# Performance work log

Measured on AMD Instinct MI355X. Metric: run time of the kernel, lower is better.

The kernel has to match this reference:

```python
import jax, jax.numpy as jnp
import numpy as np
import math

H = 16          # attention heads
NH = 4          # lact (fast-weight) heads
CHUNK = 1024    # lact_chunk_size
WIN = 1024      # sliding window
ROPE_THETA = 500000.0
BASE_LR_INV = 0.001 + math.log(-math.expm1(-0.001))  # inv_softplus(1e-3)


def rmsnorm(x, w, eps=1e-6):
    return x * jax.lax.rsqrt(jnp.mean(x * x, axis=-1, keepdims=True) + eps) * w


def rope(x, cos, sin):
    # x: [b, s, h, d]; cos/sin: [s, d//2]; non-interleaved (rotate-half) convention
    d2 = x.shape[-1] // 2
    x1, x2 = x[..., :d2], x[..., d2:]
    c = cos[None, :, None, :]
    s_ = sin[None, :, None, :]
    return jnp.concatenate([x1 * c - x2 * s_, x2 * c + x1 * s_], axis=-1)


def setup_inputs() -> dict:
    key = jax.random.key(0)
    b, s, d = 2, 2048, 2048
    fd = d // NH          # fw head dim = 512
    dh = fd               # inter_multi = 1.0
    ks = jax.random.split(key, 12)
    return {
        "hidden_states": jax.random.normal(ks[0], (b, s, d), jnp.float32),
        "Wqkv": jax.random.normal(ks[1], (3 * d, d), jnp.float32) / math.sqrt(d),
        "Wo": jax.random.normal(ks[2], (d, d), jnp.float32) / math.sqrt(d),
        "q_norm_w": jnp.ones((d,), jnp.float32),
        "k_norm_w": jnp.ones((d,), jnp.float32),
        "w0": jax.random.normal(ks[3], (NH, dh, fd), jnp.float32) / math.sqrt(fd),
        "w1": jax.random.normal(ks[4], (NH, fd, dh), jnp.float32) / math.sqrt(dh),
        "w2": jax.random.normal(ks[5], (NH, dh, fd), jnp.float32) / math.sqrt(fd),
        "lr_w": jax.random.normal(ks[6], (3 * NH, d), jnp.float32) * 0.02,
        "lr_b": jnp.zeros((3 * NH,), jnp.float32),
        "qk_scale": jnp.ones((d, 2), jnp.float32),
        "qk_offset": jnp.zeros((d, 2), jnp.float32),
        "ttt_norm_w": jnp.ones((fd,), jnp.float32),
    }


def reference(hidden_states, Wqkv, Wo, q_norm_w, k_norm_w, w0, w1, w2,
              lr_w, lr_b, qk_scale, qk_offset, ttt_norm_w):
    b, s, d = hidden_states.shape
    hd = d // H   # attn head dim
    fd = d // NH  # fw head dim

    qkv = hidden_states @ Wqkv.T
    q, k, v = jnp.split(qkv, 3, axis=-1)

    # ---------- sliding-window causal attention with RoPE ----------
    aq = rmsnorm(q, q_norm_w).reshape(b, s, H, hd)
    ak = rmsnorm(k, k_norm_w).reshape(b, s, H, hd)
    av = v.reshape(b, s, H, hd)
    inv_freq = 1.0 / (ROPE_THETA ** (jnp.arange(0, hd, 2, dtype=jnp.float32) / hd))
    ang = jnp.arange(s, dtype=jnp.float32)[:, None] * inv_freq[None, :]
    cos, sin = jnp.cos(ang), jnp.sin(ang)
    aq = rope(aq, cos, sin)
    ak = rope(ak, cos, sin)
    scores = jnp.einsum('bqhd,bkhd->bhqk', aq, ak) / math.sqrt(hd)
    i = jnp.arange(s)[:, None]
    j = jnp.arange(s)[None, :]
    mask = (j <= i) & (i - j < WIN)
    scores = jnp.where(mask[None, None], scores, -jnp.inf)
    p = jax.nn.softmax(scores, axis=-1)
    attn_out = jnp.einsum('bhqk,bkhd->bqhd', p, av).reshape(b, s, d)

    # ---------- LaCT fast-weight SwiGLU path (chunked update-then-apply) ----------
    fq = jax.nn.silu(q) * qk_scale[:, 0] + qk_offset[:, 0]
    fk = jax.nn.silu(k) * qk_scale[:, 1] + qk_offset[:, 1]
    fv = jax.nn.silu(v)
    fq = fq.reshape(b, s, NH, fd)
    fk = fk.reshape(b, s, NH, fd)
    fv = fv.reshape(b, s, NH, fd)
    # l2-normalize q/k per fw head
    fq = fq / (jnp.linalg.norm(fq, axis=-1, keepdims=True) + 1e-12)
    fk = fk / (jnp.linalg.norm(fk, axis=-1, keepdims=True) + 1e-12)
    # per-token per-head learning rates (mamba parameterization)
    lr = jax.nn.softplus(hidden_states @ lr_w.T + lr_b + BASE_LR_INV)  # [b,s,3*NH]
    lr0, lr1, lr2 = jnp.split(lr, 3, axis=-1)  # each [b,s,NH]

    nC = s // CHUNK
    BH = b * NH

    def to_chunks(x):  # [b,s,NH,fd] -> [nC, BH, CHUNK, fd]
        return x.transpose(0, 2, 1, 3).reshape(BH, nC, CHUNK, x.shape[-1]).transpose(1, 0, 2, 3)

    def lr_chunks(x):  # [b,s,NH] -> [nC, BH, CHUNK, 1]
        return x.transpose(0, 2, 1).reshape(BH, nC, CHUNK, 1).transpose(1, 0, 2, 3)

    qc, kc, vc = to_chunks(fq), to_chunks(fk), to_chunks(fv)
    l0, l1, l2 = lr_chunks(lr0), lr_chunks(lr1), lr_chunks(lr2)

    w0b = jnp.tile(w0, (b, 1, 1))  # [BH, dh, fd]
    w1b = jnp.tile(w1, (b, 1, 1))  # [BH, fd, dh]
    w2b = jnp.tile(w2, (b, 1, 1))  # [BH, dh, fd]

    def step(carry, xs):
        w0c, w1c, w2c = carry
        qi, ki, vi, li0, li1, li2 = xs
        # forward of fast net on keys
        gate = jnp.einsum('bcd,bhd->bch', ki, w0c)        # [BH,C,dh]
        hpre = jnp.einsum('bcd,bhd->bch', ki, w2c)
        hid = jax.nn.silu(gate) * hpre
        # gradient of dot-product loss  L = -sum v . f(k)  (descent direction, positive sign)
        dh_ = jnp.einsum('bco,boh->bch', vi, w1c)         # w1^T v
        dhpre = dh_ * jax.nn.silu(gate)
        sig = jax.nn.sigmoid(gate)
        dgate = dh_ * hpre * (sig * (1.0 + gate * (1.0 - sig)))
        # per-token lr-weighted updates
        w0n = w0c + jnp.einsum('bch,bcd->bhd', dgate * li0, ki)
        w2n = w2c + jnp.einsum('bch,bcd->bhd', dhpre * li2, ki)
        w1n = w1c + jnp.einsum('bco,bch->boh', vi * li1, hid)
        # apply updated fast weights to queries of this chunk
        gq = jnp.einsum('bcd,bhd->bch', qi, w0n)
        hq = jax.nn.silu(gq) * jnp.einsum('bcd,bhd->bch', qi, w2n)
        oi = jnp.einsum('bch,boh->bco', hq, w1n)
        return (w0n, w1n, w2n), oi

    _, out_c = jax.lax.scan(step, (w0b, w1b, w2b), (qc, kc, vc, l0, l1, l2))
    # [nC,BH,C,fd] -> [b,s,NH,fd]
    ttt = out_c.transpose(1, 0, 2, 3).reshape(b, NH, s, fd).transpose(0, 2, 1, 3)
    ttt = rmsnorm(ttt, ttt_norm_w).reshape(b, s, d)

    return (attn_out + ttt) @ Wo.T
```

## Files before the change

kernel.cpp:

```cpp
#include <hip/hip_runtime.h>
#include <hip/hip_bf16.h>
#include <math.h>

#define S 2048
#define NH 4
#define FD 512
#define CHUNK 1024
#define BASE_LR_INV -6.9072552373f

typedef unsigned short u16;
typedef unsigned int u32;
typedef short bhalf8 __attribute__((ext_vector_type(8)));
typedef float floatx4 __attribute__((ext_vector_type(4)));

__device__ __forceinline__ u16 f2bf(float f) {
    u32 x = __float_as_uint(f);
    return (u16)((x + 0x7FFFu + ((x >> 16) & 1u)) >> 16);
}
__device__ __forceinline__ float bf2f(u16 u) {
    return __uint_as_float(((u32)u) << 16);
}
__device__ __forceinline__ float ldval(const float* p) { return *p; }
__device__ __forceinline__ float ldval(const u16* p) { return bf2f(*p); }

__device__ __forceinline__ void gl_lds16(const u16* g, u16* l)
{
    __builtin_amdgcn_global_load_lds(
        (const __attribute__((address_space(1))) void*)g,
        (__attribute__((address_space(3))) void*)l, 16, 0, 0);
}

__global__ __launch_bounds__(256) void gemm_mfma(
    const u16* __restrict__ A, int lda, long offAo, long offAi,
    const u16* __restrict__ B, int ldb, long offBo, long offBi,
    float* __restrict__ C, int ldc, long offCo, long offCi, int K, int acc_flag)
{
    int z = blockIdx.z;
    A += (long)(z >> 2) * offAo + (long)(z & 3) * offAi;
    B += (long)(z >> 2) * offBo + (long)(z & 3) * offBi;
    C += (long)(z >> 2) * offCo + (long)(z & 3) * offCi;
    __shared__ u16 As0[128][32], Bs0[128][32];
    __shared__ u16 As1[128][32], Bs1[128][32];
    const int tid = threadIdx.x;
    const int wid = tid >> 6, lane = tid & 63;
    const int quad = lane >> 4, l15 = lane & 15;
    const int m0w = (wid >> 1) * 64, n0w = (wid & 1) * 64;
    const int row0 = blockIdx.y * 128, col0 = blockIdx.x * 128;
    const int srow = lane >> 2, scol = (lane & 3) * 8;
    const int ca = wid * 16, cb = (wid + 4) * 16;

    const u16* gA0 = &A[(long)(row0 + ca + srow) * lda + scol];
    const u16* gA1 = &A[(long)(row0 + cb + srow) * lda + scol];
    const u16* gB0 = &B[(long)(col0 + ca + srow) * ldb + scol];
    const u16* gB1 = &B[(long)(col0 + cb + srow) * ldb + scol];

    floatx4 acc[4][4];
#pragma unroll
    for (int a = 0; a < 4; ++a)
#pragma unroll
        for (int b = 0; b < 4; ++b) acc[a][b] = {0.f, 0.f, 0.f, 0.f};

#define GSTAGE(AS, BS, kk) do { \
    gl_lds16(gA0 + (kk), &AS[ca][0]); \
    gl_lds16(gA1 + (kk), &AS[cb][0]); \
    gl_lds16(gB0 + (kk), &BS[ca][0]); \
    gl_lds16(gB1 + (kk), &BS[cb][0]); } while (0)

#define GCOMP(AS, BS) do { \
    bhalf8 af[4], bf[4]; \
    _Pragma("unroll") \
    for (int mt = 0; mt < 4; ++mt) \
        af[mt] = *reinterpret_cast<const bhalf8*>(&AS[m0w + mt * 16 + l15][quad * 8]); \
    _Pragma("unroll") \
    for (int nt = 0; nt < 4; ++nt) \
        bf[nt] = *reinterpret_cast<const bhalf8*>(&BS[n0w + nt * 16 + l15][quad * 8]); \
    _Pragma("unroll") \
    for (int mt = 0; mt < 4; ++mt) \
        _Pragma("unroll") \
        for (int nt = 0; nt < 4; ++nt) \
            acc[mt][nt] = __builtin_amdgcn_mfma_f32_16x16x32_bf16( \
                af[mt], bf[nt], acc[mt][nt], 0, 0, 0); } while (0)

    const int nt = K >> 5;
    GSTAGE(As0, Bs0, 0);
    for (int t = 0; t < nt; t += 2) {
        __syncthreads();
        GSTAGE(As1, Bs1, (t + 1) * 32);
        GCOMP(As0, Bs0);
        __syncthreads();
        if (t + 2 < nt) GSTAGE(As0, Bs0, (t + 2) * 32);
        GCOMP(As1, Bs1);
    }
#undef GSTAGE
#undef GCOMP

#pragma unroll
    for (int mt = 0; mt < 4; ++mt)
#pragma unroll
        for (int nt = 0; nt < 4; ++nt) {
            int col = col0 + n0w + nt * 16 + l15;
#pragma unroll
            for (int r = 0; r < 4; ++r) {
                int row = row0 + m0w + mt * 16 + quad * 4 + r;
                long off = (long)row * ldc + col;
                float v = acc[mt][nt][r];
                C[off] = acc_flag ? (C[off] + v) : v;
            }
        }
}

__global__ __launch_bounds__(256) void gemm_mfma64(
    const u16* __restrict__ A, int lda, long offAo, long offAi,
    const u16* __restrict__ B, int ldb, long offBo, long offBi,
    float* __restrict__ C, int ldc, long offCo, long offCi, int K, int acc_flag)
{
    int z = blockIdx.z;
    A += (long)(z >> 2) * offAo + (long)(z & 3) * offAi;
    B += (long)(z >> 2) * offBo + (long)(z & 3) * offBi;
    C += (long)(z >> 2) * offCo + (long)(z & 3) * offCi;
    __shared__ u16 As0[64][32], Bs0[64][32];
    __shared__ u16 As1[64][32], Bs1[64][32];
    const int tid = threadIdx.x;
    const int wid = tid >> 6, lane = tid & 63;
    const int quad = lane >> 4, l15 = lane & 15;
    const int m0w = (wid >> 1) * 32, n0w = (wid & 1) * 32;
    const int row0 = blockIdx.y * 64, col0 = blockIdx.x * 64;
    const int srow = lane >> 2, scol = (lane & 3) * 8;
    const int ca = wid * 16;

    const u16* gA0 = &A[(long)(row0 + ca + srow) * lda + scol];
    const u16* gB0 = &B[(long)(col0 + ca + srow) * ldb + scol];

    floatx4 acc[2][2];
#pragma unroll
    for (int a = 0; a < 2; ++a)
#pragma unroll
        for (int b = 0; b < 2; ++b) acc[a][b] = {0.f, 0.f, 0.f, 0.f};

#define GSTAGE64(AS, BS, kk) do { \
    gl_lds16(gA0 + (kk), &AS[ca][0]); \
    gl_lds16(gB0 + (kk), &BS[ca][0]); } while (0)

#define GCOMP64(AS, BS) do { \
    bhalf8 af[2], bf[2]; \
    _Pragma("unroll") \
    for (int mt = 0; mt < 2; ++mt) \
        af[mt] = *reinterpret_cast<const bhalf8*>(&AS[m0w + mt * 16 + l15][quad * 8]); \
    _Pragma("unroll") \
    for (int nt = 0; nt < 2; ++nt) \
        bf[nt] = *reinterpret_cast<const bhalf8*>(&BS[n0w + nt * 16 + l15][quad * 8]); \
    _Pragma("unroll") \
    for (int mt = 0; mt < 2; ++mt) \
        _Pragma("unroll") \
        for (int nt = 0; nt < 2; ++nt) \
            acc[mt][nt] = __builtin_amdgcn_mfma_f32_16x16x32_bf16( \
                af[mt], bf[nt], acc[mt][nt], 0, 0, 0); } while (0)

    const int nt = K >> 5;
    GSTAGE64(As0, Bs0, 0);
    for (int t = 0; t < nt; t += 2) {
        __syncthreads();
        GSTAGE64(As1, Bs1, (t + 1) * 32);
        GCOMP64(As0, Bs0);
        __syncthreads();
        if (t + 2 < nt) GSTAGE64(As0, Bs0, (t + 2) * 32);
        GCOMP64(As1, Bs1);
    }
#undef GSTAGE64
#undef GCOMP64

#pragma unroll
    for (int mt = 0; mt < 2; ++mt)
#pragma unroll
        for (int nt = 0; nt < 2; ++nt) {
            int col = col0 + n0w + nt * 16 + l15;
#pragma unroll
            for (int r = 0; r < 4; ++r) {
                int row = row0 + m0w + mt * 16 + quad * 4 + r;
                long off = (long)row * ldc + col;
                float v = acc[mt][nt][r];
                C[off] = acc_flag ? (C[off] + v) : v;
            }
        }
}

__global__ __launch_bounds__(256) void cvt_bf16(
    const float* __restrict__ in, u16* __restrict__ out, long n)
{
    long i = ((long)blockIdx.x * 256 + threadIdx.x) * 4;
    if (i >= n) return;
    float4 v = *reinterpret_cast<const float4*>(&in[i]);
    ushort4 o;
    o.x = f2bf(v.x); o.y = f2bf(v.y); o.z = f2bf(v.z); o.w = f2bf(v.w);
    *reinterpret_cast<ushort4*>(&out[i]) = o;
}

__global__ __launch_bounds__(256) void cvt_pack(
    const float* __restrict__ in, u16* __restrict__ out, int half)
{
    long idx = ((long)blockIdx.x * 256 + threadIdx.x) * 4;
    int col = (int)(idx & 511);
    long r = idx >> 9;
    int row = (int)(r & 511);
    int z = (int)(r >> 9);
    float4 v = *reinterpret_cast<const float4*>(&in[idx]);
    ushort4 o;
    o.x = f2bf(v.x); o.y = f2bf(v.y); o.z = f2bf(v.z); o.w = f2bf(v.w);
    long dst = ((long)z * 1024 + half * 512 + row) * 512 + col;
    *reinterpret_cast<ushort4*>(&out[dst]) = o;
}

template <typename TIN>
__global__ __launch_bounds__(256) void transpose_cvt(
    const TIN* __restrict__ in, int ldin, long inOo, long inOi,
    u16* __restrict__ out, int ldout, long outOo, long outOi)
{
    int z = blockIdx.z;
    in  += (long)(z >> 2) * inOo + (long)(z & 3) * inOi;
    out += (long)(z >> 2) * outOo + (long)(z & 3) * outOi;
    int r0 = blockIdx.y * 64, c0 = blockIdx.x * 64;
    __shared__ float t[64][65];
    for (int i = threadIdx.x; i < 4096; i += 256) {
        int r = i >> 6, c = i & 63;
        t[r][c] = ldval(&in[(long)(r0 + r) * ldin + c0 + c]);
    }
    __syncthreads();
    for (int i = threadIdx.x; i < 4096; i += 256) {
        int r = i >> 6, c = i & 63;
        out[(long)(c0 + r) * ldout + r0 + c] = f2bf(t[c][r]);
    }
}

__global__ __launch_bounds__(256) void transpose_cvt2(
    const float* __restrict__ inA, const float* __restrict__ inB, int ldin, long inOi,
    u16* __restrict__ outA, u16* __restrict__ outB, int ldout, long outOi)
{
    int zz = blockIdx.z;
    int z = zz & 7, sel = zz >> 3;
    const float* in = (sel ? inB : inA) + (long)z * inOi;
    u16* out = (sel ? outB : outA) + (long)z * outOi;
    int r0 = blockIdx.y * 64, c0 = blockIdx.x * 64;
    __shared__ float t[64][65];
    for (int i = threadIdx.x; i < 4096; i += 256) {
        int r = i >> 6, c = i & 63;
        t[r][c] = in[(long)(r0 + r) * ldin + c0 + c];
    }
    __syncthreads();
    for (int i = threadIdx.x; i < 4096; i += 256) {
        int r = i >> 6, c = i & 63;
        out[(long)(c0 + r) * ldout + r0 + c] = f2bf(t[c][r]);
    }
}

__global__ __launch_bounds__(256) void vt_prep(
    const float* __restrict__ qkv, u16* __restrict__ vt)
{
    int z = blockIdx.z;
    int b_ = z >> 4, h = z & 15;
    int s0 = blockIdx.x * 64, d0 = blockIdx.y * 64;
    __shared__ float t[64][65];
    const float* src = &qkv[(long)(b_ * S) * 6144 + 4096 + h * 128 + d0];
    for (int i = threadIdx.x; i < 4096; i += 256) {
        int r = i >> 6, c = i & 63;
        t[r][c] = src[(long)(s0 + r) * 6144 + c];
    }
    __syncthreads();
    u16* dst = &vt[((long)z * 128 + d0) * 2048 + s0];
    for (int i = threadIdx.x; i < 4096; i += 256) {
        int r = i >> 6, c = i & 63;
        dst[(long)r * 2048 + c] = f2bf(t[c][r]);
    }
}

__global__ __launch_bounds__(256) void lr_kernel(
    const float* __restrict__ hs, const float* __restrict__ lr_w,
    const float* __restrict__ lr_b, float* __restrict__ lr)
{
    int row = blockIdx.x;
    __shared__ float hrow[2048];
    for (int i = threadIdx.x; i < 2048; i += 256) hrow[i] = hs[(long)row * 2048 + i];
    __syncthreads();
    int wid = threadIdx.x >> 6, lane = threadIdx.x & 63;
    for (int j = wid; j < 12; j += 4) {
        const float* wrow = &lr_w[(long)j * 2048];
        float ss = 0.f;
        for (int i = lane; i < 2048; i += 64) ss += hrow[i] * wrow[i];
#pragma unroll
        for (int off = 32; off > 0; off >>= 1) ss += __shfl_down(ss, off);
        if (lane == 0) {
            float x = ss + lr_b[j] + BASE_LR_INV;
            lr[(long)row * 12 + j] = (x > 20.f) ? x : log1pf(expf(x));
        }
    }
}

__global__ __launch_bounds__(256) void rmsnorm_rope(
    const float* __restrict__ qkv, int colOff, const float* __restrict__ w,
    u16* __restrict__ out)
{
    int row = blockIdx.x;
    int si = row & (S - 1);
    const float* x = &qkv[(long)row * 6144 + colOff];
    __shared__ float xn[2048];
    __shared__ float red[256];
    __shared__ float cst[64], snt[64];
    if (threadIdx.x < 64) {
        float inv_freq = powf(500000.0f, -(float)threadIdx.x / 64.0f);
        float ang = (float)si * inv_freq;
        float sn, cs;
        sincosf(ang, &sn, &cs);
        cst[threadIdx.x] = cs;
        snt[threadIdx.x] = sn;
    }
    float ss = 0.f;
    for (int i = threadIdx.x; i < 2048; i += 256) { float v = x[i]; ss += v * v; }
    red[threadIdx.x] = ss; __syncthreads();
    for (int s_ = 128; s_ > 0; s_ >>= 1) {
        if (threadIdx.x < s_) red[threadIdx.x] += red[threadIdx.x + s_];
        __syncthreads();
    }
    float scale = rsqrtf(red[0] / 2048.f + 1e-6f);
    for (int i = threadIdx.x; i < 2048; i += 256) xn[i] = x[i] * scale * w[i];
    __syncthreads();
    for (int i = threadIdx.x; i < 2048; i += 256) {
        int tt = i & 127;
        int t2 = tt & 63;
        float cs = cst[t2], sn = snt[t2];
        float v;
        if (tt < 64) v = xn[i] * cs - xn[i + 64] * sn;
        else         v = xn[i] * cs + xn[i - 64] * sn;
        out[(long)row * 2048 + i] = f2bf(v);
    }
}

__global__ __launch_bounds__(256) void attn_mfma(
    const u16* __restrict__ aq, const u16* __restrict__ ak,
    const u16* __restrict__ vt, float* __restrict__ attn_out)
{
    const int qt = blockIdx.x;
    const int h  = blockIdx.y;
    const int b_ = blockIdx.z;
    const int q0 = qt * 64;
    const int tid = threadIdx.x;
    const int wid = tid >> 6, lane = tid & 63;
    const int quad = lane >> 4, l15 = lane & 15;
    const int m0w = (wid >> 1) * 32;
    const int n0w = (wid & 1) * 32;
    const int n0v = (wid & 1) * 64;
    const float scale = 0.088388347648318447f;

    __shared__ u16  Ks[64][136];
    __shared__ float Ss[64][67];
    __shared__ u16  Ps[64][72];
    __shared__ u16  Vs[128][72];
    __shared__ float alphas[64];
    __shared__ float lsum[64];

    const long qkbase = (long)(b_ * S + q0) * 2048 + h * 128;
    const long vtbase = ((long)(b_ * 16 + h)) * 128 * 2048;

    {
        int r = tid >> 2, c = (tid & 3) * 32;
        const u16* g = &aq[qkbase + (long)r * 2048 + c];
#pragma unroll
        for (int o = 0; o < 32; o += 8)
            *reinterpret_cast<uint4*>(&Ks[r][c + o]) = *reinterpret_cast<const uint4*>(g + o);
    }
    __syncthreads();
    bhalf8 qf[2][4];
#pragma unroll
    for (int mt = 0; mt < 2; ++mt)
#pragma unroll
        for (int ks = 0; ks < 4; ++ks)
            qf[mt][ks] = *reinterpret_cast<const bhalf8*>(&Ks[m0w + mt * 16 + l15][ks * 32 + quad * 8]);
    __syncthreads();

    floatx4 oacc[2][4];
#pragma unroll
    for (int mt = 0; mt < 2; ++mt)
#pragma unroll
        for (int nt = 0; nt < 4; ++nt) oacc[mt][nt] = {0.f, 0.f, 0.f, 0.f};
    float m_i = -3.4e38f, l_i = 0.f;
    const int srow_sm = tid >> 2, scol_sm = (tid & 3) * 16;

    const int st = (qt >= 16) ? (qt - 16) : 0;
    for (int kt = st; kt <= qt; ++kt) {
        const int j0 = kt * 64;
        {
            int r = tid >> 2, c = (tid & 3) * 32;
            const u16* g = &ak[(long)(b_ * S + j0) * 2048 + h * 128 + (long)r * 2048 + c];
#pragma unroll
            for (int o = 0; o < 32; o += 8)
                *reinterpret_cast<uint4*>(&Ks[r][c + o]) = *reinterpret_cast<const uint4*>(g + o);
        }
        {
            int r = tid >> 1, c = (tid & 1) * 32;
            const u16* g = &vt[vtbase + (long)r * 2048 + j0 + c];
#pragma unroll
            for (int o = 0; o < 32; o += 8)
                *reinterpret_cast<uint4*>(&Vs[r][c + o]) = *reinterpret_cast<const uint4*>(g + o);
        }
        __syncthreads();

        floatx4 sacc[2][2];
#pragma unroll
        for (int mt = 0; mt < 2; ++mt)
#pragma unroll
            for (int nt = 0; nt < 2; ++nt) sacc[mt][nt] = {0.f, 0.f, 0.f, 0.f};
#pragma unroll
        for (int ks = 0; ks < 4; ++ks) {
            bhalf8 kf0 = *reinterpret_cast<const bhalf8*>(&Ks[n0w + l15][ks * 32 + quad * 8]);
            bhalf8 kf1 = *reinterpret_cast<const bhalf8*>(&Ks[n0w + 16 + l15][ks * 32 + quad * 8]);
            sacc[0][0] = __builtin_amdgcn_mfma_f32_16x16x32_bf16(qf[0][ks], kf0, sacc[0][0], 0, 0, 0);
            sacc[0][1] = __builtin_amdgcn_mfma_f32_16x16x32_bf16(qf[0][ks], kf1, sacc[0][1], 0, 0, 0);
            sacc[1][0] = __builtin_amdgcn_mfma_f32_16x16x32_bf16(qf[1][ks], kf0, sacc[1][0], 0, 0, 0);
            sacc[1][1] = __builtin_amdgcn_mfma_f32_16x16x32_bf16(qf[1][ks], kf1, sacc[1][1], 0, 0, 0);
        }
#pragma unroll
        for (int mt = 0; mt < 2; ++mt)
#pragma unroll
            for (int nt = 0; nt < 2; ++nt)
#pragma unroll
                for (int r = 0; r < 4; ++r) {
                    int row = m0w + mt * 16 + quad * 4 + r;
                    int col = n0w + nt * 16 + l15;
                    int i_abs = q0 + row, j_abs = j0 + col;
                    bool valid = (j_abs <= i_abs) && (i_abs - j_abs < 1024);
                    Ss[row][col] = valid ? sacc[mt][nt][r] * scale : -3.4e38f;
                }
        __syncthreads();

        {
            float sv[16];
            float mx = -3.4e38f;
#pragma unroll
            for (int j = 0; j < 16; ++j) {
                sv[j] = Ss[srow_sm][scol_sm + j];
                mx = fmaxf(mx, sv[j]);
            }
            mx = fmaxf(mx, __shfl_xor(mx, 1));
            mx = fmaxf(mx, __shfl_xor(mx, 2));
            float m_new = fmaxf(m_i, mx);
            float alpha = expf(m_i - m_new);
            float psum = 0.f;
#pragma unroll
            for (int j = 0; j < 16; ++j) {
                float p = (sv[j] > -1e30f) ? expf(sv[j] - m_new) : 0.f;
                Ps[srow_sm][scol_sm + j] = f2bf(p);
                psum += p;
            }
            psum += __shfl_xor(psum, 1);
            psum += __shfl_xor(psum, 2);
            l_i = l_i * alpha + psum;
            m_i = m_new;
            if ((tid & 3) == 0) alphas[srow_sm] = alpha;
        }
        __syncthreads();

#pragma unroll
        for (int mt = 0; mt < 2; ++mt)
#pragma unroll
            for (int r = 0; r < 4; ++r) {
                float al = alphas[m0w + mt * 16 + quad * 4 + r];
#pragma unroll
                for (int nt = 0; nt < 4; ++nt) oacc[mt][nt][r] *= al;
            }
#pragma unroll
        for (int ks = 0; ks < 2; ++ks) {
            bhalf8 pf0 = *reinterpret_cast<const bhalf8*>(&Ps[m0w + l15][ks * 32 + quad * 8]);
            bhalf8 pf1 = *reinterpret_cast<const bhalf8*>(&Ps[m0w + 16 + l15][ks * 32 + quad * 8]);
#pragma unroll
            for (int nt = 0; nt < 4; ++nt) {
                bhalf8 vf = *reinterpret_cast<const bhalf8*>(&Vs[n0v + nt * 16 + l15][ks * 32 + quad * 8]);
                oacc[0][nt] = __builtin_amdgcn_mfma_f32_16x16x32_bf16(pf0, vf, oacc[0][nt], 0, 0, 0);
                oacc[1][nt] = __builtin_amdgcn_mfma_f32_16x16x32_bf16(pf1, vf, oacc[1][nt], 0, 0, 0);
            }
        }
        __syncthreads();
    }

    if ((tid & 3) == 0) lsum[srow_sm] = l_i;
    __syncthreads();
#pragma unroll
    for (int mt = 0; mt < 2; ++mt)
#pragma unroll
        for (int r = 0; r < 4; ++r) {
            int row = m0w + mt * 16 + quad * 4 + r;
            float inv = 1.0f / lsum[row];
#pragma unroll
            for (int nt = 0; nt < 4; ++nt)
                attn_out[qkbase + (long)row * 2048 + n0v + nt * 16 + l15] = oacc[mt][nt][r] * inv;
        }
}

__global__ __launch_bounds__(128) void fqkv_kernel(
    const float* __restrict__ qkv, const float* __restrict__ qk_scale,
    const float* __restrict__ qk_offset, u16* __restrict__ fq,
    u16* __restrict__ fk, u16* __restrict__ fv)
{
    int mode = blockIdx.y;
    int bid = blockIdx.x;
    int nh = bid & 3;
    int row = bid >> 2;
    const float* x = &qkv[(long)row * 6144 + mode * 2048 + nh * 512];
    __shared__ float red[128];
    float vals[4];
    float ss = 0.f;
#pragma unroll
    for (int ii = 0; ii < 4; ++ii) {
        int i = threadIdx.x + ii * 128;
        float v = x[i];
        float sg = 1.f / (1.f + expf(-v));
        float sv = v * sg;
        if (mode < 2) {
            int dcol = nh * 512 + i;
            sv = sv * qk_scale[dcol * 2 + mode] + qk_offset[dcol * 2 + mode];
        }
        vals[ii] = sv;
        ss += sv * sv;
    }
    float invn = 1.0f;
    if (mode < 2) {
        red[threadIdx.x] = ss; __syncthreads();
        for (int s_ = 64; s_ > 0; s_ >>= 1) {
            if (threadIdx.x < s_) red[threadIdx.x] += red[threadIdx.x + s_];
            __syncthreads();
        }
        invn = 1.0f / (sqrtf(red[0]) + 1e-12f);
    }
    u16* base = (mode == 0) ? fq : (mode == 1) ? fk : fv;
    u16* o = &base[(long)row * 2048 + nh * 512];
#pragma unroll
    for (int ii = 0; ii < 4; ++ii) o[threadIdx.x + ii * 128] = f2bf(vals[ii] * invn);
}

__global__ void winit(const float* __restrict__ w0, const float* __restrict__ w1,
                      const float* __restrict__ w2, float* __restrict__ w0b,
                      float* __restrict__ w1b, float* __restrict__ w2b)
{
    long idx = (long)blockIdx.x * 256 + threadIdx.x;
    long src = ((idx >> 18) & 3) * 262144 + (idx & 262143);
    w0b[idx] = w0[src];
    w1b[idx] = w1[src];
    w2b[idx] = w2[src];
}

__global__ void scan_ew1(float* T12, float* T3, const u16* fvb,
                         const float* lr, int c0, float* T4)
{
    long idx = (long)blockIdx.x * 256 + threadIdx.x;
    int f = (int)(idx & 511);
    long r = idx >> 9;
    int ci = (int)(r & 1023);
    int z = (int)(r >> 10);
    int b_ = z >> 2, h = z & 3;
    long srow = (long)b_ * S + (long)c0 * CHUNK + ci;
    long base12 = r * 1024;
    float g = T12[base12 + f];
    float hp = T12[base12 + 512 + f];
    float dh = T3[idx];
    float sg = 1.f / (1.f + expf(-g));
    float silu_g = g * sg;
    float hid = silu_g * hp;
    float dgate = dh * hp * (sg * (1.f + g * (1.f - sg)));
    float dhpre = dh * silu_g;
    float l0 = lr[srow * 12 + h];
    float l1 = lr[srow * 12 + 4 + h];
    float l2 = lr[srow * 12 + 8 + h];
    float fvv = bf2f(fvb[srow * 2048 + h * 512 + f]);
    T12[base12 + f] = dgate * l0;
    T12[base12 + 512 + f] = dhpre * l2;
    T3[idx] = fvv * l1;
    T4[idx] = hid;
}

__global__ void scan_ew2c(const float* __restrict__ T12, u16* __restrict__ hq)
{
    long idx = (long)blockIdx.x * 256 + threadIdx.x;
    int f = (int)(idx & 511);
    long r = idx >> 9;
    long base12 = r * 1024;
    float g = T12[base12 + f];
    float h2 = T12[base12 + 512 + f];
    float v = g * (1.f / (1.f + expf(-g))) * h2;
    hq[idx] = f2bf(v);
}

__global__ __launch_bounds__(128) void ttt_norm_add(
    const float* __restrict__ ttt, const float* __restrict__ w, float* attnX)
{
    int bid = blockIdx.x;
    int h = bid & 3;
    int row = bid >> 2;
    const float* x = &ttt[(long)row * 2048 + h * 512];
    __shared__ float red[128];
    float v[4];
    float ss = 0.f;
#pragma unroll
    for (int ii = 0; ii < 4; ++ii) {
        v[ii] = x[threadIdx.x + ii * 128];
        ss += v[ii] * v[ii];
    }
    red[threadIdx.x] = ss; __syncthreads();
    for (int s_ = 64; s_ > 0; s_ >>= 1) {
        if (threadIdx.x < s_) red[threadIdx.x] += red[threadIdx.x + s_];
        __syncthreads();
    }
    float sc = rsqrtf(red[0] / 512.f + 1e-6f);
    float* o = &attnX[(long)row * 2048 + h * 512];
#pragma unroll
    for (int ii = 0; ii < 4; ++ii) {
        int i = threadIdx.x + ii * 128;
        o[i] = o[i] + v[ii] * sc * w[i];
    }
}

extern "C" void kernel_launch(void* const* d_in, const int* in_sizes, int n_in,
                              void* d_out, int out_size, void* d_ws, size_t ws_size,
                              hipStream_t stream)
{
    const float* hs        = (const float*)d_in[0];
    const float* Wqkv      = (const float*)d_in[1];
    const float* Wo        = (const float*)d_in[2];
    const float* q_norm_w  = (const float*)d_in[3];
    const float* k_norm_w  = (const float*)d_in[4];
    const float* w0        = (const float*)d_in[5];
    const float* w1        = (const float*)d_in[6];
    const float* w2        = (const float*)d_in[7];
    const float* lr_w      = (const float*)d_in[8];
    const float* lr_b      = (const float*)d_in[9];
    const float* qk_scale  = (const float*)d_in[10];
    const float* qk_offset = (const float*)d_in[11];
    const float* ttt_w     = (const float*)d_in[12];
    float* out = (float*)d_out;
    float* ws = (float*)d_ws;

    const long F_QKV = 0;
    const long F_TTT = 0;
    const long F_T1  = 8388608;
    const long F_T3  = 16777216;
    const long F_T4  = 20971520;
    const long F_AQ  = 25165824;
    const long F_AK  = 33554432;
    const long F_ATT = 41943040;
    const long F_TTa = 50331648;
    const long F_TTb = 52428800;
    const long F_W0  = 54525952;
    const long F_W1  = 56623104;
    const long F_W2  = 58720256;
    const long F_W02B= 60817408;
    const long F_W1B = 62914560;
    const long F_W1T = 63963136;
    const long F_LR  = 65011712;

    u16* hs_b   = (u16*)(ws + F_AQ);
    u16* wqkv_b = (u16*)(ws + F_AK);
    u16* aq_b   = (u16*)(ws + F_AQ);
    u16* ak_b   = (u16*)(ws + F_AK);
    u16* vt_b   = (u16*)(ws + F_AQ + 4194304);
    u16* fq_b   = (u16*)(ws + F_AQ);
    u16* fk_b   = (u16*)(ws + F_AQ + 4194304);
    u16* fv_b   = (u16*)(ws + F_AK);
    u16* hq_b   = (u16*)(ws + F_AK + 4194304);
    u16* fkt_b  = (u16*)(ws + F_AK + 6291456);
    u16* tta    = (u16*)(ws + F_TTa);
    u16* ttb    = (u16*)(ws + F_TTb);
    u16* w02b_u = (u16*)(ws + F_W02B);
    u16* w1b_u  = (u16*)(ws + F_W1B);
    u16* w1t_u  = (u16*)(ws + F_W1T);
    u16* x_b    = (u16*)(ws + F_T1);
    u16* wo_b   = (u16*)(ws + F_T3);

    cvt_bf16<<<8192, 256, 0, stream>>>(hs, hs_b, 8388608);
    cvt_bf16<<<12288, 256, 0, stream>>>(Wqkv, wqkv_b, 12582912);
    gemm_mfma<<<dim3(48, 32, 1), 256, 0, stream>>>(
        hs_b, 2048, 0, 0, wqkv_b, 2048, 0, 0, ws + F_QKV, 6144, 0, 0, 2048, 0);
    lr_kernel<<<4096, 256, 0, stream>>>(hs, lr_w, lr_b, ws + F_LR);
    rmsnorm_rope<<<4096, 256, 0, stream>>>(ws + F_QKV, 0,    q_norm_w, aq_b);
    rmsnorm_rope<<<4096, 256, 0, stream>>>(ws + F_QKV, 2048, k_norm_w, ak_b);
    vt_prep<<<dim3(32, 2, 32), 256, 0, stream>>>(ws + F_QKV, vt_b);
    attn_mfma<<<dim3(32, 16, 2), 256, 0, stream>>>(aq_b, ak_b, vt_b, ws + F_ATT);
    fqkv_kernel<<<dim3(16384, 3), 128, 0, stream>>>(
        ws + F_QKV, qk_scale, qk_offset, fq_b, fk_b, fv_b);
    winit<<<8192, 256, 0, stream>>>(w0, w1, w2, ws + F_W0, ws + F_W1, ws + F_W2);

    for (int c0 = 0; c0 < 2; ++c0) {
        const long cOff = (long)c0 * 2097152;
        cvt_pack<<<2048, 256, 0, stream>>>(ws + F_W0, w02b_u, 0);
        cvt_pack<<<2048, 256, 0, stream>>>(ws + F_W2, w02b_u, 1);
        transpose_cvt<float><<<dim3(8, 8, 8), 256, 0, stream>>>(
            ws + F_W1, 512, 1048576, 262144, w1t_u, 512, 1048576, 262144);
        transpose_cvt<u16><<<dim3(8, 16, 8), 256, 0, stream>>>(
            fk_b + cOff, 2048, 4194304, 512, fkt_b, 1024, 2097152, 524288);
        gemm_mfma<<<dim3(8, 8, 8), 256, 0, stream>>>(
            fk_b + cOff, 2048, 4194304, 512, w02b_u, 512, 2097152, 524288,
            ws + F_T1, 1024, 4194304, 1048576, 512, 0);
        gemm_mfma<<<dim3(4, 8, 8), 256, 0, stream>>>(
            fv_b + cOff, 2048, 4194304, 512, w1t_u, 512, 1048576, 262144,
            ws + F_T3, 512, 2097152, 524288, 512, 0);
        scan_ew1<<<16384, 256, 0, stream>>>(ws + F_T1, ws + F_T3, fv_b,
                                            ws + F_LR, c0, ws + F_T4);
        transpose_cvt2<<<dim3(8, 16, 16), 256, 0, stream>>>(
            ws + F_T1, ws + F_T1 + 512, 1024, 1048576, tta, ttb, 1024, 524288);
        gemm_mfma64<<<dim3(8, 8, 8), 256, 0, stream>>>(
            tta, 1024, 2097152, 524288, fkt_b, 1024, 2097152, 524288,
            ws + F_W0, 512, 1048576, 262144, 1024, 1);
        gemm_mfma64<<<dim3(8, 8, 8), 256, 0, stream>>>(
            ttb, 1024, 2097152, 524288, fkt_b, 1024, 2097152, 524288,
            ws + F_W2, 512, 1048576, 262144, 1024, 1);
        transpose_cvt2<<<dim3(8, 16, 16), 256, 0, stream>>>(
            ws + F_T3, ws + F_T4, 512, 524288, tta, ttb, 1024, 524288);
        gemm_mfma64<<<dim3(8, 8, 8), 256, 0, stream>>>(
            tta, 1024, 2097152, 524288, ttb, 1024, 2097152, 524288,
            ws + F_W1, 512, 1048576, 262144, 1024, 1);
        cvt_pack<<<2048, 256, 0, stream>>>(ws + F_W0, w02b_u, 0);
        cvt_pack<<<2048, 256, 0, stream>>>(ws + F_W2, w02b_u, 1);
        cvt_bf16<<<2048, 256, 0, stream>>>(ws + F_W1, w1b_u, 2097152);
        gemm_mfma<<<dim3(8, 8, 8), 256, 0, stream>>>(
            fq_b + cOff, 2048, 4194304, 512, w02b_u, 512, 2097152, 524288,
            ws + F_T1, 1024, 4194304, 1048576, 512, 0);
        scan_ew2c<<<16384, 256, 0, stream>>>(ws + F_T1, hq_b);
        gemm_mfma<<<dim3(4, 8, 8), 256, 0, stream>>>(
            hq_b, 512, 2097152, 524288, w1b_u, 512, 1048576, 262144,
            ws + F_TTT + cOff, 2048, 4194304, 512, 512, 0);
    }

    ttt_norm_add<<<16384, 128, 0, stream>>>(ws + F_TTT, ttt_w, ws + F_ATT);
    cvt_bf16<<<8192, 256, 0, stream>>>(ws + F_ATT, x_b, 8388608);
    cvt_bf16<<<4096, 256, 0, stream>>>(Wo, wo_b, 4194304);
    gemm_mfma<<<dim3(16, 32, 1), 256, 0, stream>>>(
        x_b, 2048, 0, 0, wo_b, 2048, 0, 0, out, 2048, 0, 0, 2048, 0);
}
```

Measured before the change: 1.007 ms.

## Fuse scan elementwise with transposes, fuse ttt norm with bf16 cast, swizzle GEMM blocks

Merges the chunk-update elementwise kernel with both transpose-convert passes into one tiled kernel that writes the four bf16 transposed operands directly through LDS. This removes two launches and the fp32 round trips through T12/T3/T4 per chunk. It also folds the final ttt rmsnorm-add into the bf16 conversion of the Wo GEMM input, dropping a read-write pass. All MFMA GEMMs now remap workgroup IDs so that consecutive tiles land on the same XCD, aiming for better L2 locality, at the cost of some index arithmetic per block.

```diff
diff --git a/kernel.cpp b/kernel.cpp
--- a/kernel.cpp
+++ b/kernel.cpp
@@ -30,12 +30,29 @@
         (__attribute__((address_space(3))) void*)l, 16, 0, 0);
 }
 
+__device__ __forceinline__ void xcd_swizzle(int& bx, int& by, int& bz)
+{
+    long gx = gridDim.x, gy = gridDim.y;
+    long nwg = gx * gy * gridDim.z;
+    long flat = blockIdx.x + gx * (blockIdx.y + gy * blockIdx.z);
+    if ((nwg & 7) == 0) {
+        long cpx = nwg >> 3;
+        flat = (flat & 7) * cpx + (flat >> 3);
+    }
+    bx = (int)(flat % gx);
+    long t = flat / gx;
+    by = (int)(t % gy);
+    bz = (int)(t / gy);
+}
+
 __global__ __launch_bounds__(256) void gemm_mfma(
     const u16* __restrict__ A, int lda, long offAo, long offAi,
     const u16* __restrict__ B, int ldb, long offBo, long offBi,
     float* __restrict__ C, int ldc, long offCo, long offCi, int K, int acc_flag)
 {
-    int z = blockIdx.z;
+    int bx, by, bz;
+    xcd_swizzle(bx, by, bz);
+    int z = bz;
     A += (long)(z >> 2) * offAo + (long)(z & 3) * offAi;
     B += (long)(z >> 2) * offBo + (long)(z & 3) * offBi;
     C += (long)(z >> 2) * offCo + (long)(z & 3) * offCi;
@@ -45,7 +62,7 @@
     const int wid = tid >> 6, lane = tid & 63;
     const int quad = lane >> 4, l15 = lane & 15;
     const int m0w = (wid >> 1) * 64, n0w = (wid & 1) * 64;
-    const int row0 = blockIdx.y * 128, col0 = blockIdx.x * 128;
+    const int row0 = by * 128, col0 = bx * 128;
     const int srow = lane >> 2, scol = (lane & 3) * 8;
     const int ca = wid * 16, cb = (wid + 4) * 16;
 
@@ -114,7 +131,9 @@
     const u16* __restrict__ B, int ldb, long offBo, long offBi,
     float* __restrict__ C, int ldc, long offCo, long offCi, int K, int acc_flag)
 {
-    int z = blockIdx.z;
+    int bx, by, bz;
+    xcd_swizzle(bx, by, bz);
+    int z = bz;
     A += (long)(z >> 2) * offAo + (long)(z & 3) * offAi;
     B += (long)(z >> 2) * offBo + (long)(z & 3) * offBi;
     C += (long)(z >> 2) * offCo + (long)(z & 3) * offCi;
@@ -124,7 +143,7 @@
     const int wid = tid >> 6, lane = tid & 63;
     const int quad = lane >> 4, l15 = lane & 15;
     const int m0w = (wid >> 1) * 32, n0w = (wid & 1) * 32;
-    const int row0 = blockIdx.y * 64, col0 = blockIdx.x * 64;
+    const int row0 = by * 64, col0 = bx * 64;
     const int srow = lane >> 2, scol = (lane & 3) * 8;
     const int ca = wid * 16;
 
@@ -231,27 +250,6 @@
     }
 }
 
-__global__ __launch_bounds__(256) void transpose_cvt2(
-    const float* __restrict__ inA, const float* __restrict__ inB, int ldin, long inOi,
-    u16* __restrict__ outA, u16* __restrict__ outB, int ldout, long outOi)
-{
-    int zz = blockIdx.z;
-    int z = zz & 7, sel = zz >> 3;
-    const float* in = (sel ? inB : inA) + (long)z * inOi;
-    u16* out = (sel ? outB : outA) + (long)z * outOi;
-    int r0 = blockIdx.y * 64, c0 = blockIdx.x * 64;
-    __shared__ float t[64][65];
-    for (int i = threadIdx.x; i < 4096; i += 256) {
-        int r = i >> 6, c = i & 63;
-        t[r][c] = in[(long)(r0 + r) * ldin + c0 + c];
-    }
-    __syncthreads();
-    for (int i = threadIdx.x; i < 4096; i += 256) {
-        int r = i >> 6, c = i & 63;
-        out[(long)(c0 + r) * ldout + r0 + c] = f2bf(t[c][r]);
-    }
-}
-
 __global__ __launch_bounds__(256) void vt_prep(
     const float* __restrict__ qkv, u16* __restrict__ vt)
 {
@@ -545,33 +543,58 @@
     w2b[idx] = w2[src];
 }
 
-__global__ void scan_ew1(float* T12, float* T3, const u16* fvb,
-                         const float* lr, int c0, float* T4)
-{
-    long idx = (long)blockIdx.x * 256 + threadIdx.x;
-    int f = (int)(idx & 511);
-    long r = idx >> 9;
-    int ci = (int)(r & 1023);
-    int z = (int)(r >> 10);
+__global__ __launch_bounds__(256) void scan_ew1t(
+    const float* __restrict__ T12, const float* __restrict__ T3,
+    const u16* __restrict__ fvb, const float* __restrict__ lr, int c0,
+    u16* __restrict__ ta, u16* __restrict__ tb,
+    u16* __restrict__ tc, u16* __restrict__ td)
+{
+    int f0 = blockIdx.x * 64, ci0 = blockIdx.y * 64, z = blockIdx.z;
     int b_ = z >> 2, h = z & 3;
-    long srow = (long)b_ * S + (long)c0 * CHUNK + ci;
-    long base12 = r * 1024;
-    float g = T12[base12 + f];
-    float hp = T12[base12 + 512 + f];
-    float dh = T3[idx];
-    float sg = 1.f / (1.f + expf(-g));
-    float silu_g = g * sg;
-    float hid = silu_g * hp;
-    float dgate = dh * hp * (sg * (1.f + g * (1.f - sg)));
-    float dhpre = dh * silu_g;
-    float l0 = lr[srow * 12 + h];
-    float l1 = lr[srow * 12 + 4 + h];
-    float l2 = lr[srow * 12 + 8 + h];
-    float fvv = bf2f(fvb[srow * 2048 + h * 512 + f]);
-    T12[base12 + f] = dgate * l0;
-    T12[base12 + 512 + f] = dhpre * l2;
-    T3[idx] = fvv * l1;
-    T4[idx] = hid;
+    __shared__ u16 la[64][66], lb[64][66], lc[64][66], ldt[64][66];
+    const int tr = threadIdx.x >> 4, tc4 = (threadIdx.x & 15) * 4;
+#pragma unroll
+    for (int it = 0; it < 4; ++it) {
+        int r = tr + it * 16;
+        long row = (long)z * 1024 + ci0 + r;
+        long srow = (long)b_ * S + (long)c0 * CHUNK + ci0 + r;
+        float4 g4  = *reinterpret_cast<const float4*>(&T12[row * 1024 + f0 + tc4]);
+        float4 hp4 = *reinterpret_cast<const float4*>(&T12[row * 1024 + 512 + f0 + tc4]);
+        float4 dh4 = *reinterpret_cast<const float4*>(&T3[row * 512 + f0 + tc4]);
+        ushort4 fv4 = *reinterpret_cast<const ushort4*>(&fvb[srow * 2048 + h * 512 + f0 + tc4]);
+        float l0 = lr[srow * 12 + h];
+        float l1 = lr[srow * 12 + 4 + h];
+        float l2 = lr[srow * 12 + 8 + h];
+        float gs[4]  = {g4.x, g4.y, g4.z, g4.w};
+        float hps[4] = {hp4.x, hp4.y, hp4.z, hp4.w};
+        float dhs[4] = {dh4.x, dh4.y, dh4.z, dh4.w};
+        u16 fvs[4]   = {fv4.x, fv4.y, fv4.z, fv4.w};
+#pragma unroll
+        for (int j = 0; j < 4; ++j) {
+            float g = gs[j], hp = hps[j], dh = dhs[j];
+            float sg = 1.f / (1.f + expf(-g));
+            float silu_g = g * sg;
+            la[r][tc4 + j]  = f2bf(dh * hp * (sg * (1.f + g * (1.f - sg))) * l0);
+            lb[r][tc4 + j]  = f2bf(dh * silu_g * l2);
+            lc[r][tc4 + j]  = f2bf(bf2f(fvs[j]) * l1);
+            ldt[r][tc4 + j] = f2bf(silu_g * hp);
+        }
+    }
+    __syncthreads();
+#pragma unroll
+    for (int it = 0; it < 4; ++it) {
+        int r = tr + it * 16;
+        long obase = ((long)z * 512 + f0 + r) * 1024 + ci0 + tc4;
+        ushort4 va, vb, vc, vd;
+        va.x = la[tc4][r];  va.y = la[tc4+1][r];  va.z = la[tc4+2][r];  va.w = la[tc4+3][r];
+        vb.x = lb[tc4][r];  vb.y = lb[tc4+1][r];  vb.z = lb[tc4+2][r];  vb.w = lb[tc4+3][r];
+        vc.x = lc[tc4][r];  vc.y = lc[tc4+1][r];  vc.z = lc[tc4+2][r];  vc.w = lc[tc4+3][r];
+        vd.x = ldt[tc4][r]; vd.y = ldt[tc4+1][r]; vd.z = ldt[tc4+2][r]; vd.w = ldt[tc4+3][r];
+        *reinterpret_cast<ushort4*>(&ta[obase]) = va;
+        *reinterpret_cast<ushort4*>(&tb[obase]) = vb;
+        *reinterpret_cast<ushort4*>(&tc[obase]) = vc;
+        *reinterpret_cast<ushort4*>(&td[obase]) = vd;
+    }
 }
 
 __global__ void scan_ew2c(const float* __restrict__ T12, u16* __restrict__ hq)
@@ -586,8 +609,9 @@
     hq[idx] = f2bf(v);
 }
 
-__global__ __launch_bounds__(128) void ttt_norm_add(
-    const float* __restrict__ ttt, const float* __restrict__ w, float* attnX)
+__global__ __launch_bounds__(128) void ttt_norm_cvt(
+    const float* __restrict__ ttt, const float* __restrict__ w,
+    const float* __restrict__ attnX, u16* __restrict__ xb)
 {
     int bid = blockIdx.x;
     int h = bid & 3;
@@ -607,11 +631,12 @@
         __syncthreads();
     }
     float sc = rsqrtf(red[0] / 512.f + 1e-6f);
-    float* o = &attnX[(long)row * 2048 + h * 512];
+    const float* a = &attnX[(long)row * 2048 + h * 512];
+    u16* o = &xb[(long)row * 2048 + h * 512];
 #pragma unroll
     for (int ii = 0; ii < 4; ++ii) {
         int i = threadIdx.x + ii * 128;
-        o[i] = o[i] + v[ii] * sc * w[i];
+        o[i] = f2bf(a[i] + v[ii] * sc * w[i]);
     }
 }
 
@@ -639,7 +664,8 @@
     const long F_TTT = 0;
     const long F_T1  = 8388608;
     const long F_T3  = 16777216;
-    const long F_T4  = 20971520;
+    const long F_TC  = 20971520;
+    const long F_TD  = 23068672;
     const long F_AQ  = 25165824;
     const long F_AK  = 33554432;
     const long F_ATT = 41943040;
@@ -665,6 +691,8 @@
     u16* fkt_b  = (u16*)(ws + F_AK + 6291456);
     u16* tta    = (u16*)(ws + F_TTa);
     u16* ttb    = (u16*)(ws + F_TTb);
+    u16* ttc    = (u16*)(ws + F_TC);
+    u16* ttd    = (u16*)(ws + F_TD);
     u16* w02b_u = (u16*)(ws + F_W02B);
     u16* w1b_u  = (u16*)(ws + F_W1B);
     u16* w1t_u  = (u16*)(ws + F_W1T);
@@ -698,20 +726,16 @@
         gemm_mfma<<<dim3(4, 8, 8), 256, 0, stream>>>(
             fv_b + cOff, 2048, 4194304, 512, w1t_u, 512, 1048576, 262144,
             ws + F_T3, 512, 2097152, 524288, 512, 0);
-        scan_ew1<<<16384, 256, 0, stream>>>(ws + F_T1, ws + F_T3, fv_b,
-                                            ws + F_LR, c0, ws + F_T4);
-        transpose_cvt2<<<dim3(8, 16, 16), 256, 0, stream>>>(
-            ws + F_T1, ws + F_T1 + 512, 1024, 1048576, tta, ttb, 1024, 524288);
+        scan_ew1t<<<dim3(8, 16, 8), 256, 0, stream>>>(
+            ws + F_T1, ws + F_T3, fv_b, ws + F_LR, c0, tta, ttb, ttc, ttd);
         gemm_mfma64<<<dim3(8, 8, 8), 256, 0, stream>>>(
             tta, 1024, 2097152, 524288, fkt_b, 1024, 2097152, 524288,
             ws + F_W0, 512, 1048576, 262144, 1024, 1);
         gemm_mfma64<<<dim3(8, 8, 8), 256, 0, stream>>>(
             ttb, 1024, 2097152, 524288, fkt_b, 1024, 2097152, 524288,
             ws + F_W2, 512, 1048576, 262144, 1024, 1);
-        transpose_cvt2<<<dim3(8, 16, 16), 256, 0, stream>>>(
-            ws + F_T3, ws + F_T4, 512, 524288, tta, ttb, 1024, 524288);
         gemm_mfma64<<<dim3(8, 8, 8), 256, 0, stream>>>(
-            tta, 1024, 2097152, 524288, ttb, 1024, 2097152, 524288,
+            ttc, 1024, 2097152, 524288, ttd, 1024, 2097152, 524288,
             ws + F_W1, 512, 1048576, 262144, 1024, 1);
         cvt_pack<<<2048, 256, 0, stream>>>(ws + F_W0, w02b_u, 0);
         cvt_pack<<<2048, 256, 0, stream>>>(ws + F_W2, w02b_u, 1);
@@ -725,8 +749,7 @@
             ws + F_TTT + cOff, 2048, 4194304, 512, 512, 0);
     }
 
-    ttt_norm_add<<<16384, 128, 0, stream>>>(ws + F_TTT, ttt_w, ws + F_ATT);
-    cvt_bf16<<<8192, 256, 0, stream>>>(ws + F_ATT, x_b, 8388608);
+    ttt_norm_cvt<<<16384, 128, 0, stream>>>(ws + F_TTT, ttt_w, ws + F_ATT, x_b);
     cvt_bf16<<<4096, 256, 0, stream>>>(Wo, wo_b, 4194304);
     gemm_mfma<<<dim3(16, 32, 1), 256, 0, stream>>>(
         x_b, 2048, 0, 0, wo_b, 2048, 0, 0, out, 2048, 0, 0, 2048, 0);
```

New measurement: 912.2 us. 1.1x faster.
